# Kernel optimization log

Hardware: AMD Instinct MI355X
Metric: run time of the kernel (lower is better)

The kernel has to match this reference:

```python
import jax, jax.numpy as jnp
import numpy as np

NODE_SIZE = 128
EDGE_SIZE = 20
CUTOFF = 5.0
N_NODES = 20000
N_EDGES = 600000


def silu(x):
    return x * jax.nn.sigmoid(x)


def setup_inputs() -> dict:
    key = jax.random.key(0)
    ks = jax.random.split(key, 20)
    d = NODE_SIZE
    inp = {
        "node_states_scalar": jax.random.normal(ks[0], (N_NODES, d), jnp.float32),
        "node_states_vector": jax.random.normal(ks[1], (N_NODES, 3, d), jnp.float32),
        "edge_states": jax.random.normal(ks[2], (N_EDGES, EDGE_SIZE), jnp.float32),
        "edge_vectors": jax.random.normal(ks[3], (N_EDGES, 3), jnp.float32),
        "edge_norms": jax.random.uniform(ks[4], (N_EDGES, 1), jnp.float32),
        "edge_index": jax.random.randint(ks[5], (N_EDGES, 2), 0, N_NODES, jnp.int64 if jax.config.jax_enable_x64 else jnp.int32),
        # parameters, stored as [in, out] so y = x @ W + b
        "Wf": jax.random.normal(ks[6], (EDGE_SIZE, 3 * d), jnp.float32) * 0.05,
        "bf": jnp.zeros((3 * d,), jnp.float32),
        "Wm1": jax.random.normal(ks[7], (d, d), jnp.float32) * 0.05,
        "bm1": jnp.zeros((d,), jnp.float32),
        "Wm2": jax.random.normal(ks[8], (d, 3 * d), jnp.float32) * 0.05,
        "bm2": jnp.zeros((3 * d,), jnp.float32),
        "WU": jax.random.normal(ks[9], (d, d), jnp.float32) * 0.05,
        "WV": jax.random.normal(ks[10], (d, d), jnp.float32) * 0.05,
        "Wa1": jax.random.normal(ks[11], (2 * d, d), jnp.float32) * 0.05,
        "ba1": jnp.zeros((d,), jnp.float32),
        "Wa2": jax.random.normal(ks[12], (d, 3 * d), jnp.float32) * 0.05,
        "ba2": jnp.zeros((3 * d,), jnp.float32),
    }
    return inp


def reference(node_states_scalar, node_states_vector, edge_states, edge_vectors,
              edge_norms, edge_index, Wf, bf, Wm1, bm1, Wm2, bm2, WU, WV,
              Wa1, ba1, Wa2, ba2):
    d = NODE_SIZE
    n = node_states_scalar.shape[0]

    # --- message function ---
    # cosine cutoff: 0.5*(cos(pi*r/cutoff)+1) for r < cutoff, else 0
    fc = 0.5 * (jnp.cos(jnp.pi * edge_norms / CUTOFF) + 1.0)
    fc = jnp.where(edge_norms < CUTOFF, fc, 0.0)                      # [E,1]
    filter_weight = (edge_states @ Wf + bf) * fc                      # [E,3d]
    scalar_output = silu(node_states_scalar @ Wm1 + bm1) @ Wm2 + bm2  # [N,3d]

    src = edge_index[:, 0]
    dst = edge_index[:, 1]
    filter_output = filter_weight * scalar_output[src]                # [E,3d]
    gate_nodes = filter_output[:, :d]
    gate_edges = filter_output[:, d:2 * d]
    messages_scalar = filter_output[:, 2 * d:]

    gated_node_vec = node_states_vector[src] * gate_nodes[:, None, :]     # [E,3,d]
    gated_edge_vec = gate_edges[:, None, :] * edge_vectors[:, :, None]    # [E,3,d]
    messages_vector = gated_node_vec + gated_edge_vec

    ds_m = jax.ops.segment_sum(messages_scalar, dst, num_segments=n)  # [N,d]
    dv_m = jax.ops.segment_sum(messages_vector, dst, num_segments=n)  # [N,3,d]

    s = node_states_scalar + ds_m
    v = node_states_vector + dv_m

    # --- node state update ---
    Uv = jnp.einsum('nvd,de->nve', v, WU)
    Vv = jnp.einsum('nvd,de->nve', v, WV)
    Vv_sq = jnp.sum(Vv ** 2, axis=1)                                  # [N,d]
    a = silu(jnp.concatenate([s, Vv_sq], axis=1) @ Wa1 + ba1) @ Wa2 + ba2
    a_ss, a_sv, a_vv = a[:, :d], a[:, d:2 * d], a[:, 2 * d:]
    ip = jnp.sum(Uv * Vv, axis=1)                                     # [N,d]

    s = s + a_ss + a_sv * ip
    v = v + a_vv[:, None, :] * Uv
    return (s, v)
```

## Files before the change

kernel.cpp:

```cpp
#include <hip/hip_runtime.h>

#define ND 128
#define ESZ 20
#define NN 20000
#define NE 600000
#define PI_F 3.14159265358979323846f
#define CUT 5.0f

using short8 = __attribute__((ext_vector_type(8))) short;
using f32x4  = __attribute__((ext_vector_type(4))) float;
using hh2    = __attribute__((ext_vector_type(2))) _Float16;

__device__ __forceinline__ float silu_f(float x) { return x / (1.0f + __expf(-x)); }

__device__ __forceinline__ unsigned short f2bf(float x) {
    unsigned u = __float_as_uint(x);
    unsigned r = (u + 0x7FFFu + ((u >> 16) & 1u)) >> 16;
    return (unsigned short)r;
}
__device__ __forceinline__ float bf2f(unsigned short h) {
    return __uint_as_float(((unsigned)h) << 16);
}
__device__ __forceinline__ unsigned pack2h(float x, float y) {
    _Float16 a = (_Float16)x, b = (_Float16)y;
    unsigned short ua = __builtin_bit_cast(unsigned short, a);
    unsigned short ub = __builtin_bit_cast(unsigned short, b);
    return (unsigned)ua | ((unsigned)ub << 16);
}
__device__ __forceinline__ float dot2u(unsigned a, hh2 b, float acc) {
    return __builtin_amdgcn_fdot2(__builtin_bit_cast(hh2, a), b, acc, false);
}

__device__ __forceinline__ void pack_w(const float* __restrict__ W,
                                       unsigned short* __restrict__ P,
                                       int s, int K, int N) {
    int k = s / N, n = s - k * N;
    int dst = ((((n >> 4) * (K >> 5) + (k >> 5)) * 64) +
               (((k >> 3) & 3) << 4) + (n & 15)) * 8 + (k & 7);
    P[dst] = f2bf(W[s]);
}

#define R0 1920000L
#define R1 (R0 + 180224L)
#define R2 (R1 + 4224L)
#define R3 (R2 + 600000L)

__global__ __launch_bounds__(256) void k_front(
    const float4* __restrict__ ns4, const float4* __restrict__ nsv4,
    const int* __restrict__ eidx,
    const float* __restrict__ Wf, const float* __restrict__ bfb,
    const float* __restrict__ Wm1, const float* __restrict__ Wm2,
    const float* __restrict__ WU, const float* __restrict__ WV,
    const float* __restrict__ Wa1, const float* __restrict__ Wa2,
    float4* __restrict__ outs4, float4* __restrict__ outv4,
    ushort4* __restrict__ nsb4, unsigned* __restrict__ gnh,
    unsigned short* __restrict__ p1, unsigned short* __restrict__ p2,
    unsigned short* __restrict__ pU, unsigned short* __restrict__ pV,
    unsigned short* __restrict__ pa1, unsigned short* __restrict__ pa2,
    unsigned* __restrict__ wfh, int* __restrict__ counts) {
    long gid = (long)blockIdx.x * 256 + threadIdx.x;
    if (gid < R0) {
        long i = gid;
        const long S4 = (long)NN * ND / 4;
        if (i < S4) {
            float4 v = ns4[i];
            outs4[i] = v;
            ushort4 h; h.x = f2bf(v.x); h.y = f2bf(v.y); h.z = f2bf(v.z); h.w = f2bf(v.w);
            nsb4[i] = h;
        }
        float4 w = nsv4[i];
        outv4[i] = w;
        unsigned short* gs = (unsigned short*)gnh;
        long b = i * 4;
        gs[(b + 0) * 2 + 1] = f2bf(w.x);
        gs[(b + 1) * 2 + 1] = f2bf(w.y);
        gs[(b + 2) * 2 + 1] = f2bf(w.z);
        gs[(b + 3) * 2 + 1] = f2bf(w.w);
    } else if (gid < R1) {
        int i = (int)(gid - R0);
        if      (i <  16384) pack_w(Wm1, p1, i,          128, 128);
        else if (i <  65536) pack_w(Wm2, p2, i - 16384,  128, 384);
        else if (i <  81920) pack_w(WU,  pU, i - 65536,  128, 128);
        else if (i <  98304) pack_w(WV,  pV, i - 81920,  128, 128);
        else if (i < 131072) pack_w(Wa1, pa1, i - 98304, 256, 128);
        else                 pack_w(Wa2, pa2, i - 131072,128, 384);
    } else if (gid < R2) {
        int j = (int)(gid - R1);
        int p = j / 384, cc = j - p * 384;
        float a = 0.f, b = 0.f;
        if (p < 10) { a = Wf[(2 * p) * 384 + cc]; b = Wf[(2 * p + 1) * 384 + cc]; }
        else if (p == 10) { a = bfb[cc]; }
        wfh[p * 384 + cc] = pack2h(a, b);
    } else if (gid < R3) {
        int e = (int)(gid - R2);
        atomicAdd(&counts[eidx[2 * e + 1]], 1);
    }
}

#define SCAN_T 1024
__global__ __launch_bounds__(SCAN_T) void k_scan(const int* __restrict__ counts,
                                                 int* __restrict__ offsets,
                                                 int* __restrict__ cursor) {
    __shared__ int part[SCAN_T];
    const int t = threadIdx.x;
    const int CPT = (NN + SCAN_T - 1) / SCAN_T;
    const int base = t * CPT;
    int sum = 0;
    for (int i = 0; i < CPT; ++i) {
        int idx = base + i;
        if (idx < NN) sum += counts[idx];
    }
    part[t] = sum;
    __syncthreads();
    for (int off = 1; off < SCAN_T; off <<= 1) {
        int v = (t >= off) ? part[t - off] : 0;
        __syncthreads();
        part[t] += v;
        __syncthreads();
    }
    int run = (t == 0) ? 0 : part[t - 1];
    for (int i = 0; i < CPT; ++i) {
        int idx = base + i;
        if (idx < NN) {
            offsets[idx] = run;
            cursor[idx] = run;
            run += counts[idx];
        }
    }
    if (t == SCAN_T - 1) offsets[NN] = run;
}

#define SCAT_B 2344
__global__ __launch_bounds__(256) void k_sm(
    const int* __restrict__ eidx, int* __restrict__ cursor,
    const float* __restrict__ es, const float* __restrict__ enorm,
    const float* __restrict__ evec, unsigned* __restrict__ rec,
    const unsigned short* __restrict__ nsb,
    const unsigned short* __restrict__ Wm1p, const float* __restrict__ bm1,
    const unsigned short* __restrict__ Wm2p, const float* __restrict__ bm2,
    unsigned* __restrict__ gnh) {
    __shared__ unsigned short lsh[4][16][136];
    if (blockIdx.x < SCAT_B) {
        int e = blockIdx.x * 256 + threadIdx.x;
        if (e < NE) {
            int s  = eidx[2 * e];
            int dd = eidx[2 * e + 1];
            float nrm = enorm[e];
            float fc = (nrm < CUT) ? 0.5f * (__cosf(PI_F * nrm * (1.0f / CUT)) + 1.0f) : 0.0f;
            const float* er = es + (long)e * ESZ;
            unsigned qv[11];
#pragma unroll
            for (int p = 0; p < 10; ++p)
                qv[p] = pack2h(er[2 * p] * fc, er[2 * p + 1] * fc);
            qv[10] = pack2h(fc, 0.f);
            float e0 = evec[3 * e + 0], e1 = evec[3 * e + 1], e2 = evec[3 * e + 2];
            int pos = atomicAdd(&cursor[dd], 1);
            uint4* rp = (uint4*)rec + (long)pos * 4;
            rp[0] = make_uint4((unsigned)s, (unsigned)dd,
                               __float_as_uint(e0), __float_as_uint(e1));
            rp[1] = make_uint4(__float_as_uint(e2), qv[0], qv[1], qv[2]);
            rp[2] = make_uint4(qv[3], qv[4], qv[5], qv[6]);
            rp[3] = make_uint4(qv[7], qv[8], qv[9], qv[10]);
        }
        return;
    }
    const int lane = threadIdx.x & 63;
    const int wv = threadIdx.x >> 6;
    const int wid = (blockIdx.x - SCAT_B) * 4 + wv;
    const int m0 = wid * 16;
    if (m0 >= NN) return;
    const int ml = lane & 15, q = lane >> 4;

    short8 a1[4];
#pragma unroll
    for (int kb = 0; kb < 4; ++kb)
        a1[kb] = *(const short8*)(nsb + (long)(m0 + ml) * ND + kb * 32 + q * 8);

#pragma unroll
    for (int nt = 0; nt < 8; ++nt) {
        float b = bm1[nt * 16 + ml];
        f32x4 acc = {b, b, b, b};
#pragma unroll
        for (int kb = 0; kb < 4; ++kb) {
            short8 bf = *(const short8*)(Wm1p + ((nt * 4 + kb) * 64 + lane) * 8);
            acc = __builtin_amdgcn_mfma_f32_16x16x32_bf16(a1[kb], bf, acc, 0, 0, 0);
        }
#pragma unroll
        for (int r = 0; r < 4; ++r)
            lsh[wv][q * 4 + r][nt * 16 + ml] = f2bf(silu_f(acc[r]));
    }
    __syncthreads();

    short8 a2[4];
#pragma unroll
    for (int kb = 0; kb < 4; ++kb)
        a2[kb] = *(const short8*)(&lsh[wv][ml][kb * 32 + q * 8]);

    unsigned short* gs = (unsigned short*)gnh;
#pragma unroll
    for (int nt = 0; nt < 24; ++nt) {
        float b = bm2[nt * 16 + ml];
        f32x4 acc = {b, b, b, b};
#pragma unroll
        for (int kb = 0; kb < 4; ++kb) {
            short8 bf = *(const short8*)(Wm2p + ((nt * 4 + kb) * 64 + lane) * 8);
            acc = __builtin_amdgcn_mfma_f32_16x16x32_bf16(a2[kb], bf, acc, 0, 0, 0);
        }
#pragma unroll
        for (int r = 0; r < 4; ++r) {
            long idx = (long)(m0 + q * 4 + r) * 384 + nt * 16 + ml;
            gs[idx * 2] = f2bf(acc[r]);
        }
    }
}

#define NGRP 7500
#define RUN 80

#define FLUSH() {                                                             \
    atomicAdd(&out_s[(long)cur_dst * ND + t], as);                            \
    atomicAdd(&out_v[(long)cur_dst * 384 + 0 * ND + t], av0);                 \
    atomicAdd(&out_v[(long)cur_dst * 384 + 1 * ND + t], av1);                 \
    atomicAdd(&out_v[(long)cur_dst * 384 + 2 * ND + t], av2);                 \
}

#define STEP(k, dk, gsrc) {                                                   \
    if (dk != cur_dst) {                                                      \
        if (cur_dst >= 0) FLUSH();                                            \
        cur_dst = dk;                                                         \
        as = 0.f; av0 = 0.f; av1 = 0.f; av2 = 0.f;                            \
    }                                                                         \
    const uint4 M0_ = pp[(k) & 1][0], M1_ = pp[(k) & 1][1],                   \
                M2_ = pp[(k) & 1][2], M3_ = pp[(k) & 1][3];                   \
    const unsigned XA_ = xr[(k) & 7][0], XB_ = xr[(k) & 7][1],                \
                   XC_ = xr[(k) & 7][2];                                      \
                                            \
    { const unsigned* pb_ = (((k) + 2 < 16) ? bc : bn) + ((((k) + 2) & 15) << 4); \
      pp[(k) & 1][0] = *(const uint4*)(pb_);                                  \
      pp[(k) & 1][1] = *(const uint4*)(pb_ + 4);                              \
      pp[(k) & 1][2] = *(const uint4*)(pb_ + 8);                              \
      pp[(k) & 1][3] = *(const uint4*)(pb_ + 12); }                           \
                                                         \
    { const unsigned* gp_ = gnh + (long)(gsrc) * 384;                         \
      xr[(k) & 7][0] = gp_[t];                                                \
      xr[(k) & 7][1] = gp_[128 + t];                                          \
      xr[(k) & 7][2] = gp_[256 + t]; }                                        \
    unsigned ea_[11] = {M1_.y, M1_.z, M1_.w, M2_.x, M2_.y, M2_.z, M2_.w,      \
                        M3_.x, M3_.y, M3_.z, M3_.w};                          \
    float f0 = 0.f, f1 = 0.f, f2 = 0.f;                                       \
    _Pragma("unroll")                                                         \
    for (int p = 0; p < 11; ++p) {                                            \
        f0 = dot2u(ea_[p], wf[p][0], f0);                                     \
        f1 = dot2u(ea_[p], wf[p][1], f1);                                     \
        f2 = dot2u(ea_[p], wf[p][2], f2);                                     \
    }                                                                         \
    f0 *= __uint_as_float(XA_ << 16);                                         \
    f1 *= __uint_as_float(XB_ << 16);                                         \
    f2 *= __uint_as_float(XC_ << 16);                                         \
    as  += f2;                                                                \
    av0 += __uint_as_float(XA_ & 0xffff0000u) * f0 + f1 * __uint_as_float(M0_.z); \
    av1 += __uint_as_float(XB_ & 0xffff0000u) * f0 + f1 * __uint_as_float(M0_.w); \
    av2 += __uint_as_float(XC_ & 0xffff0000u) * f0 + f1 * __uint_as_float(M1_.x); \
}

#define RL(v, j) __builtin_amdgcn_readlane((int)(v), (j))

__global__ __launch_bounds__(256, 3) void k_edge7(
    const unsigned* __restrict__ rec, const unsigned* __restrict__ wfh,
    const unsigned* __restrict__ gnh,
    float* __restrict__ out_s, float* __restrict__ out_v) {
    __shared__ __align__(16) unsigned eb[4][2][256];
    const int wv = threadIdx.x >> 6;
    const int lane = threadIdx.x & 63;
    const int grp = blockIdx.x * 2 + (wv >> 1);
    const int t = ((wv & 1) << 6) | lane;
    const long beg = (long)grp * RUN;

    hh2 wf[11][3];
#pragma unroll
    for (int p = 0; p < 11; ++p)
#pragma unroll
        for (int c = 0; c < 3; ++c)
            wf[p][c] = __builtin_bit_cast(hh2, wfh[p * 384 + c * 128 + t]);

    unsigned* const b0 = &eb[wv][0][0];
    unsigned* const b1 = &eb[wv][1][0];

    uint4 sA = *(const uint4*)(rec + (beg + 0)  * 16 + lane * 4);
    uint4 sB = *(const uint4*)(rec + (beg + 16) * 16 + lane * 4);
    uint4 st = *(const uint4*)(rec + (beg + 32) * 16 + lane * 4);
    *(uint4*)&b0[lane * 4] = sA;
    *(uint4*)&b1[lane * 4] = sB;
    uint2 sdC = *(const uint2*)&b0[(lane & 15) << 4];
    uint2 sdN = *(const uint2*)&b1[(lane & 15) << 4];

    uint4 pp[2][4];
    pp[0][0] = *(const uint4*)(b0 + 0);  pp[0][1] = *(const uint4*)(b0 + 4);
    pp[0][2] = *(const uint4*)(b0 + 8);  pp[0][3] = *(const uint4*)(b0 + 12);
    pp[1][0] = *(const uint4*)(b0 + 16); pp[1][1] = *(const uint4*)(b0 + 20);
    pp[1][2] = *(const uint4*)(b0 + 24); pp[1][3] = *(const uint4*)(b0 + 28);

    unsigned xr[8][3];
#define IG(j) { int s_ = RL(sdC.x, j);                                        \
                const unsigned* gp_ = gnh + (long)s_ * 384;                   \
                xr[j][0] = gp_[t]; xr[j][1] = gp_[128 + t];                   \
                xr[j][2] = gp_[256 + t]; }
    IG(0) IG(1) IG(2) IG(3) IG(4) IG(5) IG(6) IG(7)
#undef IG

    int cur_dst = -1;
    float as = 0.f, av0 = 0.f, av1 = 0.f, av2 = 0.f;

    for (int c = 0; c < 5; ++c) {
        unsigned* const bc = &eb[wv][c & 1][0];
        unsigned* const bn = &eb[wv][(c + 1) & 1][0];
        const int d0  = RL(sdC.y, 0),  d1  = RL(sdC.y, 1);
        const int d2  = RL(sdC.y, 2),  d3  = RL(sdC.y, 3);
        const int d4  = RL(sdC.y, 4),  d5  = RL(sdC.y, 5);
        const int d6  = RL(sdC.y, 6),  d7  = RL(sdC.y, 7);
        const int d8  = RL(sdC.y, 8),  d9  = RL(sdC.y, 9);
        const int d10 = RL(sdC.y, 10), d11 = RL(sdC.y, 11);
        const int d12 = RL(sdC.y, 12), d13 = RL(sdC.y, 13);
        const int d14 = RL(sdC.y, 14), d15 = RL(sdC.y, 15);
        const int s8  = RL(sdC.x, 8),  s9  = RL(sdC.x, 9);
        const int s10 = RL(sdC.x, 10), s11 = RL(sdC.x, 11);
        const int s12 = RL(sdC.x, 12), s13 = RL(sdC.x, 13);
        const int s14 = RL(sdC.x, 14), s15 = RL(sdC.x, 15);

        STEP(0, d0, s8)   STEP(1, d1, s9)   STEP(2, d2, s10)  STEP(3, d3, s11)
        STEP(4, d4, s12)  STEP(5, d5, s13)  STEP(6, d6, s14)  STEP(7, d7, s15)

        const int gm = (c < 4) ? -1 : 0;
        const int n0 = RL(sdN.x, 0) & gm, n1 = RL(sdN.x, 1) & gm;
        const int n2 = RL(sdN.x, 2) & gm, n3 = RL(sdN.x, 3) & gm;
        const int n4 = RL(sdN.x, 4) & gm, n5 = RL(sdN.x, 5) & gm;
        const int n6 = RL(sdN.x, 6) & gm, n7 = RL(sdN.x, 7) & gm;

        STEP(8,  d8,  n0)  STEP(9,  d9,  n1)  STEP(10, d10, n2) STEP(11, d11, n3)
        STEP(12, d12, n4)  STEP(13, d13, n5)  STEP(14, d14, n6) STEP(15, d15, n7)

        if (c < 4) {
            *(uint4*)&bc[lane * 4] = st;
            st = *(const uint4*)(rec + (beg + (long)(c + 3) * 16) * 16 + lane * 4);
            sdC = sdN;
            sdN = *(const uint2*)&bc[(lane & 15) << 4];
        }
    }
    FLUSH();
}

__global__ __launch_bounds__(256) void k_uvm(
    const float* __restrict__ out_v, const float* __restrict__ out_s,
    const unsigned short* __restrict__ WUp, const unsigned short* __restrict__ WVp,
    unsigned short* __restrict__ Uvh, unsigned short* __restrict__ cat,
    float* __restrict__ ipb) {
    const int lane = threadIdx.x & 63;
    const int wid = blockIdx.x * 4 + (threadIdx.x >> 6);
    const int m0 = wid * 16;
    if (m0 >= NN) return;
    const int ml = lane & 15, q = lane >> 4;

#pragma unroll
    for (int j = 0; j < 32; ++j) {
        int idx = j * 64 + lane;
        int n = m0 + (idx >> 7), c = idx & 127;
        cat[(long)n * 256 + c] = f2bf(out_s[(long)n * 128 + c]);
    }

    short8 av[3][4];
#pragma unroll
    for (int ax = 0; ax < 3; ++ax)
#pragma unroll
        for (int kb = 0; kb < 4; ++kb) {
            const float* p = out_v + (long)(m0 + ml) * 384 + ax * 128 + kb * 32 + q * 8;
            float4 x = *(const float4*)p;
            float4 y = *(const float4*)(p + 4);
            short8 s;
            s[0] = (short)f2bf(x.x); s[1] = (short)f2bf(x.y);
            s[2] = (short)f2bf(x.z); s[3] = (short)f2bf(x.w);
            s[4] = (short)f2bf(y.x); s[5] = (short)f2bf(y.y);
            s[6] = (short)f2bf(y.z); s[7] = (short)f2bf(y.w);
            av[ax][kb] = s;
        }

#pragma unroll
    for (int nt = 0; nt < 8; ++nt) {
        f32x4 u0 = {0.f,0.f,0.f,0.f}, u1 = u0, u2 = u0;
        f32x4 v0 = u0, v1 = u0, v2 = u0;
#pragma unroll
        for (int kb = 0; kb < 4; ++kb) {
            short8 bu = *(const short8*)(WUp + ((nt * 4 + kb) * 64 + lane) * 8);
            short8 bv = *(const short8*)(WVp + ((nt * 4 + kb) * 64 + lane) * 8);
            u0 = __builtin_amdgcn_mfma_f32_16x16x32_bf16(av[0][kb], bu, u0, 0, 0, 0);
            u1 = __builtin_amdgcn_mfma_f32_16x16x32_bf16(av[1][kb], bu, u1, 0, 0, 0);
            u2 = __builtin_amdgcn_mfma_f32_16x16x32_bf16(av[2][kb], bu, u2, 0, 0, 0);
            v0 = __builtin_amdgcn_mfma_f32_16x16x32_bf16(av[0][kb], bv, v0, 0, 0, 0);
            v1 = __builtin_amdgcn_mfma_f32_16x16x32_bf16(av[1][kb], bv, v1, 0, 0, 0);
            v2 = __builtin_amdgcn_mfma_f32_16x16x32_bf16(av[2][kb], bv, v2, 0, 0, 0);
        }
        const int c = nt * 16 + ml;
#pragma unroll
        for (int r = 0; r < 4; ++r) {
            long grow = m0 + q * 4 + r;
            float vs  = v0[r] * v0[r] + v1[r] * v1[r] + v2[r] * v2[r];
            float ipv = u0[r] * v0[r] + u1[r] * v1[r] + u2[r] * v2[r];
            cat[grow * 256 + 128 + c] = f2bf(vs);
            ipb[grow * 128 + c] = ipv;
            Uvh[(grow * 3 + 0) * 128 + c] = f2bf(u0[r]);
            Uvh[(grow * 3 + 1) * 128 + c] = f2bf(u1[r]);
            Uvh[(grow * 3 + 2) * 128 + c] = f2bf(u2[r]);
        }
    }
}

__global__ __launch_bounds__(256) void k_att(
    const unsigned short* __restrict__ cat,
    const unsigned short* __restrict__ Wa1p, const float* __restrict__ ba1,
    const unsigned short* __restrict__ Wa2p, const float* __restrict__ ba2,
    const float* __restrict__ ipb, const unsigned short* __restrict__ Uvh,
    float* __restrict__ out_s, float* __restrict__ out_v) {
    const int lane = threadIdx.x & 63;
    const int wv = threadIdx.x >> 6;
    const int wid = blockIdx.x * 4 + wv;
    const int m0 = wid * 16;
    if (m0 >= NN) return;
    const int ml = lane & 15, q = lane >> 4;
    __shared__ unsigned short lsh[4][16][136];

    short8 a1[8];
#pragma unroll
    for (int kb = 0; kb < 8; ++kb)
        a1[kb] = *(const short8*)(cat + (long)(m0 + ml) * 256 + kb * 32 + q * 8);

#pragma unroll
    for (int nt = 0; nt < 8; ++nt) {
        float b = ba1[nt * 16 + ml];
        f32x4 acc = {b, b, b, b};
#pragma unroll
        for (int kb = 0; kb < 8; ++kb) {
            short8 bf = *(const short8*)(Wa1p + ((nt * 8 + kb) * 64 + lane) * 8);
            acc = __builtin_amdgcn_mfma_f32_16x16x32_bf16(a1[kb], bf, acc, 0, 0, 0);
        }
#pragma unroll
        for (int r = 0; r < 4; ++r)
            lsh[wv][q * 4 + r][nt * 16 + ml] = f2bf(silu_f(acc[r]));
    }
    __syncthreads();

    short8 h[4];
#pragma unroll
    for (int kb = 0; kb < 4; ++kb)
        h[kb] = *(const short8*)(&lsh[wv][ml][kb * 32 + q * 8]);

#pragma unroll
    for (int nt = 0; nt < 8; ++nt) {
        float b0 = ba2[nt * 16 + ml];
        float b1 = ba2[128 + nt * 16 + ml];
        f32x4 aS = {b0, b0, b0, b0};
        f32x4 aG = {b1, b1, b1, b1};
#pragma unroll
        for (int kb = 0; kb < 4; ++kb) {
            short8 bS = *(const short8*)(Wa2p + (((nt) * 4 + kb) * 64 + lane) * 8);
            short8 bG = *(const short8*)(Wa2p + (((nt + 8) * 4 + kb) * 64 + lane) * 8);
            aS = __builtin_amdgcn_mfma_f32_16x16x32_bf16(h[kb], bS, aS, 0, 0, 0);
            aG = __builtin_amdgcn_mfma_f32_16x16x32_bf16(h[kb], bG, aG, 0, 0, 0);
        }
#pragma unroll
        for (int r = 0; r < 4; ++r) {
            long grow = m0 + q * 4 + r;
            long o = grow * 128 + nt * 16 + ml;
            float ipv = ipb[o];
            out_s[o] = out_s[o] + aS[r] + aG[r] * ipv;
        }
    }

#pragma unroll
    for (int nt = 0; nt < 8; ++nt) {
        float b2 = ba2[256 + nt * 16 + ml];
        f32x4 aV = {b2, b2, b2, b2};
#pragma unroll
        for (int kb = 0; kb < 4; ++kb) {
            short8 bV = *(const short8*)(Wa2p + (((nt + 16) * 4 + kb) * 64 + lane) * 8);
            aV = __builtin_amdgcn_mfma_f32_16x16x32_bf16(h[kb], bV, aV, 0, 0, 0);
        }
#pragma unroll
        for (int r = 0; r < 4; ++r) {
            long grow = m0 + q * 4 + r;
            int c = nt * 16 + ml;
#pragma unroll
            for (int ax = 0; ax < 3; ++ax) {
                float u = bf2f(Uvh[(grow * 3 + ax) * 128 + c]);
                long o = grow * 384 + ax * 128 + c;
                out_v[o] = out_v[o] + aV[r] * u;
            }
        }
    }
}

extern "C" void kernel_launch(void* const* d_in, const int* in_sizes, int n_in,
                              void* d_out, int out_size, void* d_ws, size_t ws_size,
                              hipStream_t stream) {
    const float* ns    = (const float*)d_in[0];
    const float* nsv   = (const float*)d_in[1];
    const float* es    = (const float*)d_in[2];
    const float* evec  = (const float*)d_in[3];
    const float* enorm = (const float*)d_in[4];
    const int*   eidx  = (const int*)d_in[5];
    const float* Wf    = (const float*)d_in[6];
    const float* bfb   = (const float*)d_in[7];
    const float* Wm1   = (const float*)d_in[8];
    const float* bm1   = (const float*)d_in[9];
    const float* Wm2   = (const float*)d_in[10];
    const float* bm2   = (const float*)d_in[11];
    const float* WU    = (const float*)d_in[12];
    const float* WV    = (const float*)d_in[13];
    const float* Wa1   = (const float*)d_in[14];
    const float* ba1   = (const float*)d_in[15];
    const float* Wa2   = (const float*)d_in[16];
    const float* ba2   = (const float*)d_in[17];

    float* out_s = (float*)d_out;
    float* out_v = out_s + (size_t)NN * ND;

    char* w = (char*)d_ws;
    unsigned short* p1  = (unsigned short*)(w + 0);
    unsigned short* p2  = (unsigned short*)(w + 32768);
    unsigned short* pU  = (unsigned short*)(w + 131072);
    unsigned short* pV  = (unsigned short*)(w + 163840);
    unsigned short* pa1 = (unsigned short*)(w + 196608);
    unsigned short* pa2 = (unsigned short*)(w + 262144);
    unsigned* wfh = (unsigned*)(w + 360448);
    int* counts = (int*)(w + 377344);
    int* offs   = (int*)(w + 457344);
    int* cursor = (int*)(w + 537408);
    unsigned* rec = (unsigned*)(w + 617408);
    char* u0 = w + 39024576;
    unsigned* gnh       = (unsigned*)(u0);
    unsigned short* nsb = (unsigned short*)(u0 + 30720000);
    unsigned short* Uvh = (unsigned short*)(u0);
    unsigned short* cat = (unsigned short*)(u0 + 15360000);
    float*          ipb = (float*)(u0 + 25600000);

    hipMemsetAsync(counts, 0, (size_t)NN * sizeof(int), stream);
    hipMemsetAsync(rec + (size_t)NE * 16, 0, 112 * 64, stream);
    k_front<<<(int)((R3 + 255) / 256), 256, 0, stream>>>(
        (const float4*)ns, (const float4*)nsv, eidx, Wf, bfb,
        Wm1, Wm2, WU, WV, Wa1, Wa2,
        (float4*)out_s, (float4*)out_v, (ushort4*)nsb, gnh,
        p1, p2, pU, pV, pa1, pa2, wfh, counts);
    k_scan<<<1, SCAN_T, 0, stream>>>(counts, offs, cursor);
    k_sm<<<SCAT_B + 313, 256, 0, stream>>>(eidx, cursor, es, enorm, evec, rec,
                                           nsb, p1, bm1, p2, bm2, gnh);
    k_edge7<<<NGRP / 2, 256, 0, stream>>>(rec, wfh, gnh, out_s, out_v);
    k_uvm<<<313, 256, 0, stream>>>(out_v, out_s, pU, pV, Uvh, cat, ipb);
    k_att<<<313, 256, 0, stream>>>(cat, pa1, ba1, pa2, ba2, ipb, Uvh,
                                   out_s, out_v);
}
```

Before: 517.4 us.

## Fuse node-update kernels and batch edge atomics through shared-memory slots

Merges the Uv/Vv projection kernel and the attention/update kernel into one tail kernel. The concatenated features and hidden activations now stay in per-wave LDS, and the inner product and bf16 Uv values stay in registers, instead of round-tripping through global workspace buffers. In the edge kernel, per-destination partial sums are staged in shared-memory slots and flushed to global atomics in batches of eight. This is meant to move the atomic traffic off the critical inner loop. The costs are higher register and LDS pressure in the tail kernel, which may lower occupancy, and extra LDS traffic in the edge kernel.

```diff
diff --git a/kernel.cpp b/kernel.cpp
--- a/kernel.cpp
+++ b/kernel.cpp
@@ -20,6 +20,9 @@
 }
 __device__ __forceinline__ float bf2f(unsigned short h) {
     return __uint_as_float(((unsigned)h) << 16);
+}
+__device__ __forceinline__ unsigned pack2bf(float x, float y) {
+    return (unsigned)f2bf(x) | ((unsigned)f2bf(y) << 16);
 }
 __device__ __forceinline__ unsigned pack2h(float x, float y) {
     _Float16 a = (_Float16)x, b = (_Float16)y;
@@ -216,18 +219,12 @@
 
 #define NGRP 7500
 #define RUN 80
-
-#define FLUSH() {                                                             \
-    atomicAdd(&out_s[(long)cur_dst * ND + t], as);                            \
-    atomicAdd(&out_v[(long)cur_dst * 384 + 0 * ND + t], av0);                 \
-    atomicAdd(&out_v[(long)cur_dst * 384 + 1 * ND + t], av1);                 \
-    atomicAdd(&out_v[(long)cur_dst * 384 + 2 * ND + t], av2);                 \
-}
+#define SLOTS 8
 
 #define STEP(k, dk, gsrc) {                                                   \
-    if (dk != cur_dst) {                                                      \
-        if (cur_dst >= 0) FLUSH();                                            \
-        cur_dst = dk;                                                         \
+    if ((dk) != cur_dst) {                                                    \
+        PUSH();                                                               \
+        cur_dst = (dk);                                                       \
         as = 0.f; av0 = 0.f; av1 = 0.f; av2 = 0.f;                            \
     }                                                                         \
     const uint4 M0_ = pp[(k) & 1][0], M1_ = pp[(k) & 1][1],                   \
@@ -265,11 +262,13 @@
 
 #define RL(v, j) __builtin_amdgcn_readlane((int)(v), (j))
 
-__global__ __launch_bounds__(256, 3) void k_edge7(
+__global__ __launch_bounds__(256, 3) void k_edge8(
     const unsigned* __restrict__ rec, const unsigned* __restrict__ wfh,
     const unsigned* __restrict__ gnh,
     float* __restrict__ out_s, float* __restrict__ out_v) {
     __shared__ __align__(16) unsigned eb[4][2][256];
+    __shared__ float fsl[4][SLOTS][4][64];
+    __shared__ int dsl[4][SLOTS];
     const int wv = threadIdx.x >> 6;
     const int lane = threadIdx.x & 63;
     const int grp = blockIdx.x * 2 + (wv >> 1);
@@ -309,7 +308,30 @@
 #undef IG
 
     int cur_dst = -1;
+    int nseg = 0;
     float as = 0.f, av0 = 0.f, av1 = 0.f, av2 = 0.f;
+
+    auto DRAIN = [&]() {
+        for (int i = 0; i < nseg; ++i) {
+            int d = dsl[wv][i];
+            atomicAdd(&out_s[(long)d * ND + t],            fsl[wv][i][0][lane]);
+            atomicAdd(&out_v[(long)d * 384 + 0 * ND + t],  fsl[wv][i][1][lane]);
+            atomicAdd(&out_v[(long)d * 384 + 1 * ND + t],  fsl[wv][i][2][lane]);
+            atomicAdd(&out_v[(long)d * 384 + 2 * ND + t],  fsl[wv][i][3][lane]);
+        }
+        nseg = 0;
+    };
+    auto PUSH = [&]() {
+        if (cur_dst >= 0) {
+            fsl[wv][nseg][0][lane] = as;
+            fsl[wv][nseg][1][lane] = av0;
+            fsl[wv][nseg][2][lane] = av1;
+            fsl[wv][nseg][3][lane] = av2;
+            if (lane == 0) dsl[wv][nseg] = cur_dst;
+            ++nseg;
+            if (nseg == SLOTS) DRAIN();
+        }
+    };
 
     for (int c = 0; c < 5; ++c) {
         unsigned* const bc = &eb[wv][c & 1][0];
@@ -346,25 +368,30 @@
             sdN = *(const uint2*)&bc[(lane & 15) << 4];
         }
     }
-    FLUSH();
-}
-
-__global__ __launch_bounds__(256) void k_uvm(
-    const float* __restrict__ out_v, const float* __restrict__ out_s,
+    PUSH();
+    DRAIN();
+}
+
+__global__ __launch_bounds__(256) void k_tail(
     const unsigned short* __restrict__ WUp, const unsigned short* __restrict__ WVp,
-    unsigned short* __restrict__ Uvh, unsigned short* __restrict__ cat,
-    float* __restrict__ ipb) {
+    const unsigned short* __restrict__ Wa1p, const float* __restrict__ ba1,
+    const unsigned short* __restrict__ Wa2p, const float* __restrict__ ba2,
+    float* __restrict__ out_s, float* __restrict__ out_v) {
     const int lane = threadIdx.x & 63;
-    const int wid = blockIdx.x * 4 + (threadIdx.x >> 6);
+    const int wv = threadIdx.x >> 6;
+    const int wid = blockIdx.x * 4 + wv;
     const int m0 = wid * 16;
     if (m0 >= NN) return;
     const int ml = lane & 15, q = lane >> 4;
-
-#pragma unroll
-    for (int j = 0; j < 32; ++j) {
+    __shared__ unsigned short ct[4][16][264];
+    __shared__ unsigned short hl[4][16][136];
+
+#pragma unroll
+    for (int j = 0; j < 16; ++j) {
         int idx = j * 64 + lane;
-        int n = m0 + (idx >> 7), c = idx & 127;
-        cat[(long)n * 256 + c] = f2bf(out_s[(long)n * 128 + c]);
+        int n = idx >> 6, c2 = idx & 63;
+        float2 sv = *(const float2*)(out_s + (long)(m0 + n) * 128 + c2 * 2);
+        *(unsigned*)&ct[wv][n][c2 * 2] = pack2bf(sv.x, sv.y);
     }
 
     short8 av[3][4];
@@ -383,6 +410,8 @@
             av[ax][kb] = s;
         }
 
+    f32x4 ipr[8];
+    unsigned upk[8][3][2];
 #pragma unroll
     for (int nt = 0; nt < 8; ++nt) {
         f32x4 u0 = {0.f,0.f,0.f,0.f}, u1 = u0, u2 = u0;
@@ -401,36 +430,19 @@
         const int c = nt * 16 + ml;
 #pragma unroll
         for (int r = 0; r < 4; ++r) {
-            long grow = m0 + q * 4 + r;
             float vs  = v0[r] * v0[r] + v1[r] * v1[r] + v2[r] * v2[r];
-            float ipv = u0[r] * v0[r] + u1[r] * v1[r] + u2[r] * v2[r];
-            cat[grow * 256 + 128 + c] = f2bf(vs);
-            ipb[grow * 128 + c] = ipv;
-            Uvh[(grow * 3 + 0) * 128 + c] = f2bf(u0[r]);
-            Uvh[(grow * 3 + 1) * 128 + c] = f2bf(u1[r]);
-            Uvh[(grow * 3 + 2) * 128 + c] = f2bf(u2[r]);
-        }
-    }
-}
-
-__global__ __launch_bounds__(256) void k_att(
-    const unsigned short* __restrict__ cat,
-    const unsigned short* __restrict__ Wa1p, const float* __restrict__ ba1,
-    const unsigned short* __restrict__ Wa2p, const float* __restrict__ ba2,
-    const float* __restrict__ ipb, const unsigned short* __restrict__ Uvh,
-    float* __restrict__ out_s, float* __restrict__ out_v) {
-    const int lane = threadIdx.x & 63;
-    const int wv = threadIdx.x >> 6;
-    const int wid = blockIdx.x * 4 + wv;
-    const int m0 = wid * 16;
-    if (m0 >= NN) return;
-    const int ml = lane & 15, q = lane >> 4;
-    __shared__ unsigned short lsh[4][16][136];
+            ct[wv][q * 4 + r][128 + c] = f2bf(vs);
+            ipr[nt][r] = u0[r] * v0[r] + u1[r] * v1[r] + u2[r] * v2[r];
+        }
+        upk[nt][0][0] = pack2bf(u0[0], u0[1]); upk[nt][0][1] = pack2bf(u0[2], u0[3]);
+        upk[nt][1][0] = pack2bf(u1[0], u1[1]); upk[nt][1][1] = pack2bf(u1[2], u1[3]);
+        upk[nt][2][0] = pack2bf(u2[0], u2[1]); upk[nt][2][1] = pack2bf(u2[2], u2[3]);
+    }
 
     short8 a1[8];
 #pragma unroll
     for (int kb = 0; kb < 8; ++kb)
-        a1[kb] = *(const short8*)(cat + (long)(m0 + ml) * 256 + kb * 32 + q * 8);
+        a1[kb] = *(const short8*)(&ct[wv][ml][kb * 32 + q * 8]);
 
 #pragma unroll
     for (int nt = 0; nt < 8; ++nt) {
@@ -443,14 +455,13 @@
         }
 #pragma unroll
         for (int r = 0; r < 4; ++r)
-            lsh[wv][q * 4 + r][nt * 16 + ml] = f2bf(silu_f(acc[r]));
-    }
-    __syncthreads();
+            hl[wv][q * 4 + r][nt * 16 + ml] = f2bf(silu_f(acc[r]));
+    }
 
     short8 h[4];
 #pragma unroll
     for (int kb = 0; kb < 4; ++kb)
-        h[kb] = *(const short8*)(&lsh[wv][ml][kb * 32 + q * 8]);
+        h[kb] = *(const short8*)(&hl[wv][ml][kb * 32 + q * 8]);
 
 #pragma unroll
     for (int nt = 0; nt < 8; ++nt) {
@@ -469,8 +480,7 @@
         for (int r = 0; r < 4; ++r) {
             long grow = m0 + q * 4 + r;
             long o = grow * 128 + nt * 16 + ml;
-            float ipv = ipb[o];
-            out_s[o] = out_s[o] + aS[r] + aG[r] * ipv;
+            out_s[o] = out_s[o] + aS[r] + aG[r] * ipr[nt][r];
         }
     }
 
@@ -489,9 +499,11 @@
             int c = nt * 16 + ml;
 #pragma unroll
             for (int ax = 0; ax < 3; ++ax) {
-                float u = bf2f(Uvh[(grow * 3 + ax) * 128 + c]);
+                unsigned pk = upk[nt][ax][r >> 1];
+                unsigned short uh = (r & 1) ? (unsigned short)(pk >> 16)
+                                            : (unsigned short)(pk & 0xffffu);
                 long o = grow * 384 + ax * 128 + c;
-                out_v[o] = out_v[o] + aV[r] * u;
+                out_v[o] = out_v[o] + aV[r] * bf2f(uh);
             }
         }
     }
@@ -537,9 +549,6 @@
     char* u0 = w + 39024576;
     unsigned* gnh       = (unsigned*)(u0);
     unsigned short* nsb = (unsigned short*)(u0 + 30720000);
-    unsigned short* Uvh = (unsigned short*)(u0);
-    unsigned short* cat = (unsigned short*)(u0 + 15360000);
-    float*          ipb = (float*)(u0 + 25600000);
 
     hipMemsetAsync(counts, 0, (size_t)NN * sizeof(int), stream);
     hipMemsetAsync(rec + (size_t)NE * 16, 0, 112 * 64, stream);
@@ -551,8 +560,6 @@
     k_scan<<<1, SCAN_T, 0, stream>>>(counts, offs, cursor);
     k_sm<<<SCAT_B + 313, 256, 0, stream>>>(eidx, cursor, es, enorm, evec, rec,
                                            nsb, p1, bm1, p2, bm2, gnh);
-    k_edge7<<<NGRP / 2, 256, 0, stream>>>(rec, wfh, gnh, out_s, out_v);
-    k_uvm<<<313, 256, 0, stream>>>(out_v, out_s, pU, pV, Uvh, cat, ipb);
-    k_att<<<313, 256, 0, stream>>>(cat, pa1, ba1, pa2, ba2, ipb, Uvh,
-                                   out_s, out_v);
-}
+    k_edge8<<<NGRP / 2, 256, 0, stream>>>(rec, wfh, gnh, out_s, out_v);
+    k_tail<<<313, 256, 0, stream>>>(pU, pV, pa1, ba1, pa2, ba2, out_s, out_v);
+}
```

New measurement: 482.2 us. 1.07x faster.
